# Optimization experiments

Measured on AMD Instinct MI355X. Metric: run time of the kernel, lower is better.

## Reference

```python
import jax, jax.numpy as jnp
import numpy as np

D_MODEL = 1024
D_FF = 4096
N_EXPERTS = 8
TOP_K = 2
BATCH = 4
SEQ = 2048


def setup_inputs() -> dict:
    key = jax.random.key(0)
    k0, k1, k2, k3, k4 = jax.random.split(key, 5)
    x = jax.random.normal(k0, (BATCH, SEQ, D_MODEL), dtype=jnp.float32)
    # MLP router: Linear(d,d) + bias, Tanh, Linear(d,E) no bias
    Wg1 = jax.random.normal(k1, (D_MODEL, D_MODEL), dtype=jnp.float32) * (1.0 / np.sqrt(D_MODEL))
    bg1 = jnp.zeros((D_MODEL,), dtype=jnp.float32)
    Wg2 = jax.random.normal(k2, (D_MODEL, N_EXPERTS), dtype=jnp.float32) * (1.0 / np.sqrt(D_MODEL))
    # ParallelExperts weights: [E, in, out] (bias=False)
    W1 = jax.random.normal(k3, (N_EXPERTS, D_MODEL, D_FF), dtype=jnp.float32) * 0.02
    W2 = jax.random.normal(k4, (N_EXPERTS, D_FF, D_MODEL), dtype=jnp.float32) * 0.02
    return {"x": x, "Wg1": Wg1, "bg1": bg1, "Wg2": Wg2, "W1": W1, "W2": W2}


def reference(x, Wg1, bg1, Wg2, W1, W2):
    B, L, d = x.shape
    T = B * L
    xf = x.reshape(T, d)

    # ---- top-k gating (eval mode: no noise, no dropout, no skip_mask) ----
    logits = jnp.tanh(xf @ Wg1 + bg1) @ Wg2          # [T, E]
    probs = jax.nn.softmax(logits, axis=-1)          # [T, E]
    top_k_gates, top_k_idx = jax.lax.top_k(probs, TOP_K)
    top_k_gates = top_k_gates / (top_k_gates.sum(axis=-1, keepdims=True) + 1e-6)
    # dense gate matrix: gates[t, e] = normalized gate if e selected for token t else 0
    gates = jnp.zeros_like(probs).at[jnp.arange(T)[:, None], top_k_idx].set(top_k_gates)

    # ---- expert FFNs + gate-weighted combine ----
    # Mathematically identical to scatter-dispatch/grouped-GEMM/index_add combine:
    # y_t = sum_e gates[t,e] * (gelu(x_t @ W1_e) @ W2_e); unselected experts have gate 0.
    # Scan over the small fixed expert axis to avoid an [E, T, d_ff] intermediate.
    def body(y, scanned):
        w1, w2, g = scanned                           # [d,h], [h,d], [T]
        h = jax.nn.gelu(xf @ w1)                      # [T, h]
        return y + (h @ w2) * g[:, None], None

    y0 = jnp.zeros((T, d), dtype=x.dtype)
    y, _ = jax.lax.scan(body, y0, (W1, W2, gates.T))

    # all aux-loss coefficients default to 0 -> loss is 0
    loss = jnp.asarray(0.0, dtype=x.dtype)
    return y.reshape(B, L, d), loss
```

## Files before the change

kernel.cpp:

```cpp
#include <hip/hip_runtime.h>
#include <hip/hip_bf16.h>
#include <math.h>

#define T_TOK 8192
#define DM 1024
#define DFF 4096
#define NE 8
#define HROWS 16512
#define MAX_TILES 136
#define TPX 17

#define NB_SPLIT (T_TOK * DM / 4 / 256)
#define NB_TW1 ((DFF / 32) * (DM / 32) * NE)
#define NB_TW2 ((DM / 32) * (DFF / 32) * NE)
#define NB_TSW ((DM / 32) * (DM / 32))
#define NB_ZY 8193
#define NB_ZLOG 64
#define NB_ZMETA 1
#define NB_PREP (NB_SPLIT + NB_TW1 + NB_TW2 + NB_TSW + NB_ZY + NB_ZLOG + NB_ZMETA)

typedef __attribute__((ext_vector_type(8))) short bf16x8;
typedef __attribute__((ext_vector_type(4))) float f32x4;
typedef __attribute__((ext_vector_type(8))) _Float16 f16x8;
typedef __attribute__((ext_vector_type(4))) _Float16 f16x4;

__device__ __forceinline__ void async16(const void* g, void* l) {
  __builtin_amdgcn_global_load_lds((const __attribute__((address_space(1))) void*)g,
                                   (__attribute__((address_space(3))) void*)l, 16, 0, 0);
}

__device__ __forceinline__ unsigned short f2b(float f) {
  __hip_bfloat16 h = __float2bfloat16(f);
  return *reinterpret_cast<unsigned short*>(&h);
}

__device__ __forceinline__ float tanh_fast(float z) {
  return 1.f - 2.f / (__expf(2.f * z) + 1.f);
}

__device__ __forceinline__ float gelu_fast(float v) {
  float u = v + 0.044715f * v * v * v;
  return v / (1.f + __expf(-1.5957691216057308f * u));
}

__global__ __launch_bounds__(256) void prep_all_kernel(
    const float* __restrict__ x, unsigned short* __restrict__ xb,
    _Float16* __restrict__ xh, _Float16* __restrict__ xl,
    const float* __restrict__ W1, unsigned short* __restrict__ w1t,
    const float* __restrict__ W2, unsigned short* __restrict__ w2t,
    const float* __restrict__ Wg1, _Float16* __restrict__ wth, _Float16* __restrict__ wtl,
    float* __restrict__ y, int out_size, float* __restrict__ logits, int* __restrict__ meta) {
  __shared__ float tile[32][33];
  const int b = blockIdx.x;
  const int tid = threadIdx.x;

  if (b < NB_SPLIT) {
    int i = b * 256 + tid;
    float4 v = reinterpret_cast<const float4*>(x)[i];
    ushort4 ob;
    f16x4 oh, ol;
    float f, hf;
    f = v.x; oh[0] = (_Float16)f; hf = (float)oh[0]; ol[0] = (_Float16)((f - hf) * 2048.0f); ob.x = f2b(f);
    f = v.y; oh[1] = (_Float16)f; hf = (float)oh[1]; ol[1] = (_Float16)((f - hf) * 2048.0f); ob.y = f2b(f);
    f = v.z; oh[2] = (_Float16)f; hf = (float)oh[2]; ol[2] = (_Float16)((f - hf) * 2048.0f); ob.z = f2b(f);
    f = v.w; oh[3] = (_Float16)f; hf = (float)oh[3]; ol[3] = (_Float16)((f - hf) * 2048.0f); ob.w = f2b(f);
    reinterpret_cast<ushort4*>(xb)[i] = ob;
    reinterpret_cast<f16x4*>(xh)[i] = oh;
    reinterpret_cast<f16x4*>(xl)[i] = ol;
    return;
  }

  if (b >= NB_SPLIT + NB_TW1 + NB_TW2 + NB_TSW) {
    int zb = b - (NB_SPLIT + NB_TW1 + NB_TW2 + NB_TSW);
    if (zb < NB_ZY) {
      int i4 = zb * 256 + tid;
      if ((i4 + 1) * 4 <= out_size) {
        reinterpret_cast<float4*>(y)[i4] = make_float4(0.f, 0.f, 0.f, 0.f);
      } else {
#pragma unroll
        for (int k = 0; k < 4; k++) {
          int idx = i4 * 4 + k;
          if (idx < out_size) y[idx] = 0.f;
        }
      }
    } else if (zb < NB_ZY + NB_ZLOG) {
      int i4 = (zb - NB_ZY) * 256 + tid;
      reinterpret_cast<float4*>(logits)[i4] = make_float4(0.f, 0.f, 0.f, 0.f);
    } else {
      if (tid < 16) meta[tid] = 0;
    }
    return;
  }

  const int tx = tid & 31, ty = tid >> 5;

  if (b < NB_SPLIT + NB_TW1) {
    int idx = b - NB_SPLIT;
    int e = idx >> 12, rem = idx & 4095;
    int by = rem >> 7, bx = rem & 127;
    int r0 = by * 32, c0 = bx * 32;
    const float* src = W1 + (size_t)e * DM * DFF;
    unsigned short* dst = w1t + (size_t)e * DM * DFF;
#pragma unroll
    for (int i = 0; i < 32; i += 8) tile[ty + i][tx] = src[(size_t)(r0 + ty + i) * DFF + c0 + tx];
    __syncthreads();
#pragma unroll
    for (int i = 0; i < 32; i += 8) dst[(size_t)(c0 + ty + i) * DM + r0 + tx] = f2b(tile[tx][ty + i]);
    return;
  }

  if (b < NB_SPLIT + NB_TW1 + NB_TW2) {
    int idx = b - NB_SPLIT - NB_TW1;
    int e = idx >> 12, rem = idx & 4095;
    int by = rem >> 5, bx = rem & 31;
    int r0 = by * 32, c0 = bx * 32;
    const float* src = W2 + (size_t)e * DFF * DM;
    unsigned short* dst = w2t + (size_t)e * DFF * DM;
#pragma unroll
    for (int i = 0; i < 32; i += 8) tile[ty + i][tx] = src[(size_t)(r0 + ty + i) * DM + c0 + tx];
    __syncthreads();
#pragma unroll
    for (int i = 0; i < 32; i += 8) dst[(size_t)(c0 + ty + i) * DFF + r0 + tx] = f2b(tile[tx][ty + i]);
    return;
  }

  {
    int idx = b - NB_SPLIT - NB_TW1 - NB_TW2;
    int by = idx >> 5, bx = idx & 31;
    int r0 = by * 32, c0 = bx * 32;
#pragma unroll
    for (int i = 0; i < 32; i += 8) tile[ty + i][tx] = Wg1[(size_t)(r0 + ty + i) * DM + c0 + tx];
    __syncthreads();
#pragma unroll
    for (int i = 0; i < 32; i += 8) {
      float f = tile[tx][ty + i];
      _Float16 h = (_Float16)f;
      size_t idx2 = (size_t)(c0 + ty + i) * DM + r0 + tx;
      wth[idx2] = h;
      wtl[idx2] = (_Float16)((f - (float)h) * 2048.0f);
    }
  }
}

__global__ __launch_bounds__(256) void router_mfma_kernel(
    const _Float16* __restrict__ xh, const _Float16* __restrict__ xl,
    const _Float16* __restrict__ wth, const _Float16* __restrict__ wtl,
    const float* __restrict__ bg1, const float* __restrict__ Wg2,
    float* __restrict__ logits) {
  __shared__ __align__(16) char AB[2][32768];
  __shared__ float lgt[128 * 2 * NE];

  const int tid = threadIdx.x;
  const int lane = tid & 63;
  const int w = tid >> 6;
  const int n0 = blockIdx.x * 128, m0 = blockIdx.y * 128;

  const int r0 = w * 16 + (lane >> 2);
  const int r1 = r0 + 64;
  const int sp = lane & 3;
  const int k0s = (sp ^ ((r0 >> 1) & 3)) * 8;
  const int k1s = (sp ^ ((r1 >> 1) & 3)) * 8;

  const _Float16* gAh0 = xh + (size_t)(m0 + r0) * DM + k0s;
  const _Float16* gAh1 = xh + (size_t)(m0 + r1) * DM + k1s;
  const _Float16* gAl0 = xl + (size_t)(m0 + r0) * DM + k0s;
  const _Float16* gAl1 = xl + (size_t)(m0 + r1) * DM + k1s;
  const _Float16* gBh0 = wth + (size_t)(n0 + r0) * DM + k0s;
  const _Float16* gBh1 = wth + (size_t)(n0 + r1) * DM + k1s;
  const _Float16* gBl0 = wtl + (size_t)(n0 + r0) * DM + k0s;
  const _Float16* gBl1 = wtl + (size_t)(n0 + r1) * DM + k1s;

  const int wr = (w >> 1) * 64, wc = (w & 1) * 64;
  const int l15 = lane & 15, ls = lane >> 4;

  f32x4 zero = {0.f, 0.f, 0.f, 0.f};
  f32x4 acc_hh[4][4], acc_c[4][4];
#pragma unroll
  for (int i = 0; i < 4; i++)
#pragma unroll
    for (int j = 0; j < 4; j++) { acc_hh[i][j] = zero; acc_c[i][j] = zero; }

  auto stage = [&](int buf, int kt) {
    char* b = &AB[buf][0] + w * 1024;
    async16(gAh0 + kt, b);
    async16(gAh1 + kt, b + 4096);
    async16(gAl0 + kt, b + 8192);
    async16(gAl1 + kt, b + 8192 + 4096);
    async16(gBh0 + kt, b + 16384);
    async16(gBh1 + kt, b + 16384 + 4096);
    async16(gBl0 + kt, b + 24576);
    async16(gBl1 + kt, b + 24576 + 4096);
  };
  auto computeTile = [&](int cur) {
    const char* base = &AB[cur][0];
    f16x8 ah[4], bh[4], tmp[4];
#pragma unroll
    for (int i = 0; i < 4; i++) {
      int ar = wr + i * 16 + l15;
      ah[i] = *(const f16x8*)(base + ar * 64 + ((ls ^ ((ar >> 1) & 3)) << 4));
    }
#pragma unroll
    for (int j = 0; j < 4; j++) {
      int br = wc + j * 16 + l15;
      bh[j] = *(const f16x8*)(base + 16384 + br * 64 + ((ls ^ ((br >> 1) & 3)) << 4));
    }
    __builtin_amdgcn_s_setprio(1);
#pragma unroll
    for (int i = 0; i < 4; i++)
#pragma unroll
      for (int j = 0; j < 4; j++)
        acc_hh[i][j] = __builtin_amdgcn_mfma_f32_16x16x32_f16(ah[i], bh[j], acc_hh[i][j], 0, 0, 0);
    __builtin_amdgcn_s_setprio(0);
#pragma unroll
    for (int j = 0; j < 4; j++) {
      int br = wc + j * 16 + l15;
      tmp[j] = *(const f16x8*)(base + 24576 + br * 64 + ((ls ^ ((br >> 1) & 3)) << 4));
    }
    __builtin_amdgcn_s_setprio(1);
#pragma unroll
    for (int i = 0; i < 4; i++)
#pragma unroll
      for (int j = 0; j < 4; j++)
        acc_c[i][j] = __builtin_amdgcn_mfma_f32_16x16x32_f16(ah[i], tmp[j], acc_c[i][j], 0, 0, 0);
    __builtin_amdgcn_s_setprio(0);
#pragma unroll
    for (int i = 0; i < 4; i++) {
      int ar = wr + i * 16 + l15;
      tmp[i] = *(const f16x8*)(base + 8192 + ar * 64 + ((ls ^ ((ar >> 1) & 3)) << 4));
    }
    __builtin_amdgcn_s_setprio(1);
#pragma unroll
    for (int i = 0; i < 4; i++)
#pragma unroll
      for (int j = 0; j < 4; j++)
        acc_c[i][j] = __builtin_amdgcn_mfma_f32_16x16x32_f16(tmp[i], bh[j], acc_c[i][j], 0, 0, 0);
    __builtin_amdgcn_s_setprio(0);
  };

  const int NIT = DM / 32;
  stage(0, 0);
  __syncthreads();
#pragma unroll 2
  for (int t = 0; t < NIT - 1; t++) {
    const int cur = t & 1;
    stage(cur ^ 1, (t + 1) * 32);
    computeTile(cur);
    __syncthreads();
  }
  computeTile((NIT - 1) & 1);

  float w2r[4][8];
  float bias[4];
#pragma unroll
  for (int j = 0; j < 4; j++) {
    int gn = n0 + wc + j * 16 + l15;
    bias[j] = bg1[gn];
    float4 u = *(const float4*)(Wg2 + (size_t)gn * NE);
    float4 v = *(const float4*)(Wg2 + (size_t)gn * NE + 4);
    w2r[j][0] = u.x; w2r[j][1] = u.y; w2r[j][2] = u.z; w2r[j][3] = u.w;
    w2r[j][4] = v.x; w2r[j][5] = v.y; w2r[j][6] = v.z; w2r[j][7] = v.w;
  }
  const float inv2k = 1.0f / 2048.0f;
  const int half = wc >> 6;
  const bool b3 = (l15 & 8) != 0, b2 = (l15 & 4) != 0, b1 = (l15 & 2) != 0;
#pragma unroll
  for (int i = 0; i < 4; i++) {
#pragma unroll
    for (int r = 0; r < 4; r++) {
      float s[8] = {0.f, 0.f, 0.f, 0.f, 0.f, 0.f, 0.f, 0.f};
#pragma unroll
      for (int j = 0; j < 4; j++) {
        float hv = tanh_fast(acc_hh[i][j][r] + acc_c[i][j][r] * inv2k + bias[j]);
#pragma unroll
        for (int e = 0; e < NE; e++) s[e] = fmaf(hv, w2r[j][e], s[e]);
      }
      float t4_[4], t2_[2], t1_;
#pragma unroll
      for (int q = 0; q < 4; q++) {
        float snd = b3 ? s[q] : s[q + 4];
        float rcv = __shfl_xor(snd, 8);
        t4_[q] = (b3 ? s[q + 4] : s[q]) + rcv;
      }
#pragma unroll
      for (int q = 0; q < 2; q++) {
        float snd = b2 ? t4_[q] : t4_[q + 2];
        float rcv = __shfl_xor(snd, 4);
        t2_[q] = (b2 ? t4_[q + 2] : t4_[q]) + rcv;
      }
      {
        float snd = b1 ? t2_[0] : t2_[1];
        float rcv = __shfl_xor(snd, 2);
        t1_ = (b1 ? t2_[1] : t2_[0]) + rcv;
      }
      t1_ += __shfl_xor(t1_, 1);
      int m = wr + i * 16 + ls * 4 + r;
      if (!(l15 & 1)) lgt[m * (2 * NE) + half * NE + (l15 >> 1)] = t1_;
    }
  }
  __syncthreads();
#pragma unroll
  for (int q = 0; q < 4; q++) {
    int idx = tid * 4 + q;
    int m = idx >> 3, e = idx & 7;
    float v = lgt[m * (2 * NE) + e] + lgt[m * (2 * NE) + NE + e];
    atomicAdd(&logits[(size_t)(m0 + m) * NE + e], v);
  }
}

__global__ __launch_bounds__(256) void topk_small_kernel(
    const float* __restrict__ logits, int* __restrict__ tIdx, float* __restrict__ tGate,
    int* __restrict__ counts) {
  __shared__ int lc[NE];
  const int tid = threadIdx.x;
  if (tid < NE) lc[tid] = 0;
  __syncthreads();
  int t = blockIdx.x * 256 + tid;
  float p[NE];
  float4 p0 = *(const float4*)(logits + (size_t)t * NE);
  float4 p1 = *(const float4*)(logits + (size_t)t * NE + 4);
  p[0] = p0.x; p[1] = p0.y; p[2] = p0.z; p[3] = p0.w;
  p[4] = p1.x; p[5] = p1.y; p[6] = p1.z; p[7] = p1.w;
  float v1 = -1e30f, v2 = -1e30f; int i1 = 0, i2 = 1;
#pragma unroll
  for (int e = 0; e < NE; e++) {
    float v = p[e];
    if (v > v1) { v2 = v1; i2 = i1; v1 = v; i1 = e; }
    else if (v > v2) { v2 = v; i2 = e; }
  }
  float mx = v1;
  float s = 0.f;
#pragma unroll
  for (int e = 0; e < NE; e++) s += __expf(p[e] - mx);
  float inv = 1.f / s;
  float g1 = __expf(p[i1] - mx) * inv;
  float g2 = __expf(p[i2] - mx) * inv;
  float den = 1.f / (g1 + g2 + 1e-6f);
  tIdx[2 * t] = i1; tIdx[2 * t + 1] = i2;
  tGate[2 * t] = g1 * den; tGate[2 * t + 1] = g2 * den;
  atomicAdd(&lc[i1], 1);
  atomicAdd(&lc[i2], 1);
  __syncthreads();
  if (tid < NE) atomicAdd(&counts[tid], lc[tid]);
}

__global__ void build_tiles_kernel(const int* __restrict__ counts, int* __restrict__ offsets,
                                   int4* __restrict__ desc, int* __restrict__ nTiles) {
  if (threadIdx.x != 0 || blockIdx.x != 0) return;
  int off = 0, nt = 0;
  for (int e = 0; e < NE; e++) {
    offsets[e] = off;
    int c = counts[e];
    if (c < 0) c = 0;
    if (c > 2 * T_TOK) c = 2 * T_TOK;
    for (int r = 0; r < c && nt < MAX_TILES; r += 128) {
      int v = c - r; if (v > 128) v = 128;
      desc[nt++] = make_int4(e, off + r, v, 0);
    }
    off += c;
    if (off > 2 * T_TOK) off = 2 * T_TOK;
  }
  offsets[NE] = off;
  *nTiles = nt;
}

__global__ void scatter_kernel(const int* __restrict__ tIdx, const float* __restrict__ tGate,
                               const int* __restrict__ offsets, int* __restrict__ fill,
                               int* __restrict__ tokList, float* __restrict__ gateList) {
  int id = blockIdx.x * blockDim.x + threadIdx.x;
  if (id >= 2 * T_TOK) return;
  int e = tIdx[id] & 7;
  int pos = atomicAdd(&fill[e], 1);
  int row = offsets[e] + pos;
  if (row < 0 || row >= 2 * T_TOK) return;
  tokList[row] = id >> 1;
  gateList[row] = tGate[id];
}

__global__ __launch_bounds__(256) void ffn1_kernel(
    const unsigned short* __restrict__ xb, const unsigned short* __restrict__ w1t,
    const int* __restrict__ tokList, const int4* __restrict__ desc,
    const int* __restrict__ nTiles, unsigned short* __restrict__ h) {
  const int g = blockIdx.x;
  const int tileIdx = (g & 7) * TPX + ((g >> 3) % TPX);
  const int nb = g / (8 * TPX);
  if (tileIdx >= *nTiles) return;
  int4 d = desc[tileIdx];
  const int e = d.x, rowStart = d.y, valid = d.z;
  const int n0 = nb * 128;

  __shared__ __align__(16) char AB[3][16384];

  const int tid = threadIdx.x;
  const int lane = tid & 63;
  const int w = tid >> 6;

  const int r0 = w * 16 + (lane >> 2);
  const int r1 = r0 + 64;
  const int sp = lane & 3;
  const int k0s = (sp ^ ((r0 >> 1) & 3)) * 8;
  const int k1s = (sp ^ ((r1 >> 1) & 3)) * 8;

  const unsigned short* gA0 = xb + (size_t)(tokList[rowStart + r0] & (T_TOK - 1)) * DM + k0s;
  const unsigned short* gA1 = xb + (size_t)(tokList[rowStart + r1] & (T_TOK - 1)) * DM + k1s;
  const unsigned short* gB0 = w1t + ((size_t)e * DFF + n0 + r0) * DM + k0s;
  const unsigned short* gB1 = w1t + ((size_t)e * DFF + n0 + r1) * DM + k1s;

  const int wr = (w >> 1) * 64, wc = (w & 1) * 64;
  const int l15 = lane & 15, ls = lane >> 4;

  f32x4 zero = {0.f, 0.f, 0.f, 0.f};
  f32x4 acc[4][4];
#pragma unroll
  for (int i = 0; i < 4; i++)
#pragma unroll
    for (int j = 0; j < 4; j++) acc[i][j] = zero;

  auto stage = [&](int buf, int kt) {
    char* dA = &AB[buf][0] + w * 1024;
    char* dB = dA + 8192;
    async16(gA0 + kt, dA);
    async16(gA1 + kt, dA + 4096);
    async16(gB0 + kt, dB);
    async16(gB1 + kt, dB + 4096);
  };
  auto computeTile = [&](int cur) {
    const char* rA = &AB[cur][0];
    const char* rB = rA + 8192;
    bf16x8 af[4], bfv[4];
#pragma unroll
    for (int i = 0; i < 4; i++) {
      int ar = wr + i * 16 + l15;
      af[i] = *(const bf16x8*)(rA + ar * 64 + ((ls ^ ((ar >> 1) & 3)) << 4));
    }
#pragma unroll
    for (int j = 0; j < 4; j++) {
      int br = wc + j * 16 + l15;
      bfv[j] = *(const bf16x8*)(rB + br * 64 + ((ls ^ ((br >> 1) & 3)) << 4));
    }
    __builtin_amdgcn_s_setprio(1);
#pragma unroll
    for (int i = 0; i < 4; i++)
#pragma unroll
      for (int j = 0; j < 4; j++)
        acc[i][j] = __builtin_amdgcn_mfma_f32_16x16x32_bf16(af[i], bfv[j], acc[i][j], 0, 0, 0);
    __builtin_amdgcn_s_setprio(0);
  };

  const int NIT = DM / 32;
  stage(0, 0);
  stage(1, 32);
  int cur = 0, stg = 2;
  for (int t = 0; t < NIT; t++) {
    if (t < NIT - 1) asm volatile("s_waitcnt vmcnt(4)" ::: "memory");
    else             asm volatile("s_waitcnt vmcnt(0)" ::: "memory");
    __builtin_amdgcn_s_barrier();
    __builtin_amdgcn_sched_barrier(0);
    if (t < NIT - 2) {
      stage(stg, (t + 2) * 32);
      stg = (stg == 2) ? 0 : stg + 1;
    }
    computeTile(cur);
    cur = (cur == 2) ? 0 : cur + 1;
  }

#pragma unroll
  for (int i = 0; i < 4; i++) {
#pragma unroll
    for (int r = 0; r < 4; r++) {
      int m = wr + i * 16 + ls * 4 + r;
      if (m < valid) {
        size_t base = (size_t)(rowStart + m) * DFF + n0 + wc;
#pragma unroll
        for (int j = 0; j < 4; j++) {
          h[base + j * 16 + l15] = f2b(gelu_fast(acc[i][j][r]));
        }
      }
    }
  }
}

__global__ __launch_bounds__(256) void ffn2_kernel(
    const unsigned short* __restrict__ h, const unsigned short* __restrict__ w2t,
    const int* __restrict__ tokList, const float* __restrict__ gateList,
    const int4* __restrict__ desc, const int* __restrict__ nTiles,
    float* __restrict__ y) {
  const int g = blockIdx.x;
  const int tileIdx = (g & 7) * TPX + ((g >> 3) % TPX);
  const int nb = g / (8 * TPX);
  if (tileIdx >= *nTiles) return;
  int4 d = desc[tileIdx];
  const int e = d.x, rowStart = d.y, valid = d.z;
  const int n0 = nb * 128;

  __shared__ __align__(16) char AB[3][16384];

  const int tid = threadIdx.x;
  const int lane = tid & 63;
  const int w = tid >> 6;

  const int r0 = w * 16 + (lane >> 2);
  const int r1 = r0 + 64;
  const int sp = lane & 3;
  const int k0s = (sp ^ ((r0 >> 1) & 3)) * 8;
  const int k1s = (sp ^ ((r1 >> 1) & 3)) * 8;

  const unsigned short* gA0 = h + (size_t)(rowStart + r0) * DFF + k0s;
  const unsigned short* gA1 = h + (size_t)(rowStart + r1) * DFF + k1s;
  const unsigned short* gB0 = w2t + ((size_t)e * DM + n0 + r0) * DFF + k0s;
  const unsigned short* gB1 = w2t + ((size_t)e * DM + n0 + r1) * DFF + k1s;

  const int wr = (w >> 1) * 64, wc = (w & 1) * 64;
  const int l15 = lane & 15, ls = lane >> 4;

  f32x4 zero = {0.f, 0.f, 0.f, 0.f};
  f32x4 acc[4][4];
#pragma unroll
  for (int i = 0; i < 4; i++)
#pragma unroll
    for (int j = 0; j < 4; j++) acc[i][j] = zero;

  auto stage = [&](int buf, int kt) {
    char* dA = &AB[buf][0] + w * 1024;
    char* dB = dA + 8192;
    async16(gA0 + kt, dA);
    async16(gA1 + kt, dA + 4096);
    async16(gB0 + kt, dB);
    async16(gB1 + kt, dB + 4096);
  };
  auto computeTile = [&](int cur) {
    const char* rA = &AB[cur][0];
    const char* rB = rA + 8192;
    bf16x8 af[4], bfv[4];
#pragma unroll
    for (int i = 0; i < 4; i++) {
      int ar = wr + i * 16 + l15;
      af[i] = *(const bf16x8*)(rA + ar * 64 + ((ls ^ ((ar >> 1) & 3)) << 4));
    }
#pragma unroll
    for (int j = 0; j < 4; j++) {
      int br = wc + j * 16 + l15;
      bfv[j] = *(const bf16x8*)(rB + br * 64 + ((ls ^ ((br >> 1) & 3)) << 4));
    }
    __builtin_amdgcn_s_setprio(1);
#pragma unroll
    for (int i = 0; i < 4; i++)
#pragma unroll
      for (int j = 0; j < 4; j++)
        acc[i][j] = __builtin_amdgcn_mfma_f32_16x16x32_bf16(af[i], bfv[j], acc[i][j], 0, 0, 0);
    __builtin_amdgcn_s_setprio(0);
  };

  const int NIT = DFF / 32;
  stage(0, 0);
  stage(1, 32);
  int cur = 0, stg = 2;
  for (int t = 0; t < NIT; t++) {
    if (t < NIT - 1) asm volatile("s_waitcnt vmcnt(4)" ::: "memory");
    else             asm volatile("s_waitcnt vmcnt(0)" ::: "memory");
    __builtin_amdgcn_s_barrier();
    __builtin_amdgcn_sched_barrier(0);
    if (t < NIT - 2) {
      stage(stg, (t + 2) * 32);
      stg = (stg == 2) ? 0 : stg + 1;
    }
    computeTile(cur);
    cur = (cur == 2) ? 0 : cur + 1;
  }

#pragma unroll
  for (int i = 0; i < 4; i++) {
#pragma unroll
    for (int r = 0; r < 4; r++) {
      int m = wr + i * 16 + ls * 4 + r;
      if (m < valid) {
        int row = rowStart + m;
        int tok = tokList[row] & (T_TOK - 1);
        float g2 = gateList[row];
        float* yr = y + (size_t)tok * DM + n0 + wc;
#pragma unroll
        for (int j = 0; j < 4; j++) {
          atomicAdd(&yr[j * 16 + l15], g2 * acc[i][j][r]);
        }
      }
    }
  }
}

extern "C" void kernel_launch(void* const* d_in, const int* in_sizes, int n_in,
                              void* d_out, int out_size, void* d_ws, size_t ws_size,
                              hipStream_t stream) {
  const float* x   = (const float*)d_in[0];
  const float* Wg1 = (const float*)d_in[1];
  const float* bg1 = (const float*)d_in[2];
  const float* Wg2 = (const float*)d_in[3];
  const float* W1  = (const float*)d_in[4];
  const float* W2  = (const float*)d_in[5];
  float* y = (float*)d_out;
  char* ws = (char*)d_ws;

  const size_t SZ_W1T = (size_t)NE * DFF * DM * 2;
  const size_t OFF_W1T = 0;
  const size_t OFF_W2T = OFF_W1T + SZ_W1T;
  const size_t OFF_XB  = OFF_W2T + SZ_W1T;
  const size_t OFF_H   = OFF_XB + (size_t)T_TOK * DM * 2;
  const size_t OFF_TOK = OFF_H + (size_t)HROWS * DFF * 2;
  const size_t OFF_GATE = OFF_TOK + (size_t)HROWS * 4;
  const size_t OFF_TIDX = OFF_GATE + (size_t)HROWS * 4;
  const size_t OFF_TG   = OFF_TIDX + (size_t)2 * T_TOK * 4;
  const size_t OFF_LOG  = OFF_TG + (size_t)2 * T_TOK * 4;
  const size_t OFF_META = OFF_LOG + (size_t)T_TOK * NE * 4;
  const size_t NEED = OFF_META + 4096;

  const size_t OFF_XH  = OFF_H;
  const size_t OFF_XL  = OFF_XH + (size_t)T_TOK * DM * 2;
  const size_t OFF_WTH = OFF_XL + (size_t)T_TOK * DM * 2;
  const size_t OFF_WTL = OFF_WTH + (size_t)DM * DM * 2;

  if (ws_size < NEED) {
    hipMemsetAsync(d_out, 0, (size_t)out_size * 4, stream);
    return;
  }

  unsigned short* w1t = (unsigned short*)(ws + OFF_W1T);
  unsigned short* w2t = (unsigned short*)(ws + OFF_W2T);
  unsigned short* xb  = (unsigned short*)(ws + OFF_XB);
  unsigned short* h   = (unsigned short*)(ws + OFF_H);
  _Float16* xh        = (_Float16*)(ws + OFF_XH);
  _Float16* xl        = (_Float16*)(ws + OFF_XL);
  _Float16* wth       = (_Float16*)(ws + OFF_WTH);
  _Float16* wtl       = (_Float16*)(ws + OFF_WTL);
  int* tokList        = (int*)(ws + OFF_TOK);
  float* gateList     = (float*)(ws + OFF_GATE);
  int* tIdx           = (int*)(ws + OFF_TIDX);
  float* tGate        = (float*)(ws + OFF_TG);
  float* logits       = (float*)(ws + OFF_LOG);
  int* meta           = (int*)(ws + OFF_META);
  int* counts         = (int*)(ws + OFF_META);
  int* fill           = (int*)(ws + OFF_META + 32);
  int* offsets        = (int*)(ws + OFF_META + 64);
  int* nTiles         = (int*)(ws + OFF_META + 128);
  int4* desc          = (int4*)(ws + OFF_META + 160);

  prep_all_kernel<<<dim3(NB_PREP), dim3(256), 0, stream>>>(
      x, xb, xh, xl, W1, w1t, W2, w2t, Wg1, wth, wtl, y, out_size, logits, meta);

  router_mfma_kernel<<<dim3(DM / 128, T_TOK / 128), dim3(256), 0, stream>>>(xh, xl, wth, wtl,
                                                                            bg1, Wg2, logits);
  topk_small_kernel<<<dim3(T_TOK / 256), dim3(256), 0, stream>>>(logits, tIdx, tGate, counts);
  build_tiles_kernel<<<dim3(1), dim3(64), 0, stream>>>(counts, offsets, desc, nTiles);
  scatter_kernel<<<dim3((2 * T_TOK) / 256), dim3(256), 0, stream>>>(tIdx, tGate, offsets, fill,
                                                                    tokList, gateList);

  ffn1_kernel<<<dim3((DFF / 128) * MAX_TILES), dim3(256), 0, stream>>>(xb, w1t, tokList, desc,
                                                                       nTiles, h);
  ffn2_kernel<<<dim3((DM / 128) * MAX_TILES), dim3(256), 0, stream>>>(h, w2t, tokList, gateList,
                                                                      desc, nTiles, y);
}
```

Measured before the change: 674.8 us.

## Widen expert GEMM tiles to 128x256 and split FFN2 K dimension in two

Both expert GEMM kernels now compute 128x256 output tiles instead of 128x128. Each wave holds a 64x128 accumulator, and the B-operand staging is widened to four async loads per stage. The aim is more MFMA work per LDS load and less redundant A-operand traffic. FFN2 additionally splits its 4096-long K reduction into two halves accumulated through the existing atomics, so the grid keeps enough blocks. The costs are doubled accumulator registers (lower occupancy), larger LDS use, and twice as many atomic adds on y.

```diff
diff --git a/kernel.cpp b/kernel.cpp
--- a/kernel.cpp
+++ b/kernel.cpp
@@ -386,9 +386,9 @@
   if (tileIdx >= *nTiles) return;
   int4 d = desc[tileIdx];
   const int e = d.x, rowStart = d.y, valid = d.z;
-  const int n0 = nb * 128;
-
-  __shared__ __align__(16) char AB[3][16384];
+  const int n0 = nb * 256;
+
+  __shared__ __align__(16) char AB[3][24576];
 
   const int tid = threadIdx.x;
   const int lane = tid & 63;
@@ -397,43 +397,44 @@
   const int r0 = w * 16 + (lane >> 2);
   const int r1 = r0 + 64;
   const int sp = lane & 3;
-  const int k0s = (sp ^ ((r0 >> 1) & 3)) * 8;
-  const int k1s = (sp ^ ((r1 >> 1) & 3)) * 8;
-
-  const unsigned short* gA0 = xb + (size_t)(tokList[rowStart + r0] & (T_TOK - 1)) * DM + k0s;
-  const unsigned short* gA1 = xb + (size_t)(tokList[rowStart + r1] & (T_TOK - 1)) * DM + k1s;
-  const unsigned short* gB0 = w1t + ((size_t)e * DFF + n0 + r0) * DM + k0s;
-  const unsigned short* gB1 = w1t + ((size_t)e * DFF + n0 + r1) * DM + k1s;
-
-  const int wr = (w >> 1) * 64, wc = (w & 1) * 64;
+  const int ks = (sp ^ ((r0 >> 1) & 3)) * 8;
+
+  const unsigned short* gA0 = xb + (size_t)(tokList[rowStart + r0] & (T_TOK - 1)) * DM + ks;
+  const unsigned short* gA1 = xb + (size_t)(tokList[rowStart + r1] & (T_TOK - 1)) * DM + ks;
+  const unsigned short* gB[4];
+#pragma unroll
+  for (int i = 0; i < 4; i++)
+    gB[i] = w1t + ((size_t)e * DFF + n0 + i * 64 + r0) * DM + ks;
+
+  const int wr = (w >> 1) * 64, wc = (w & 1) * 128;
   const int l15 = lane & 15, ls = lane >> 4;
 
   f32x4 zero = {0.f, 0.f, 0.f, 0.f};
-  f32x4 acc[4][4];
+  f32x4 acc[4][8];
 #pragma unroll
   for (int i = 0; i < 4; i++)
 #pragma unroll
-    for (int j = 0; j < 4; j++) acc[i][j] = zero;
+    for (int j = 0; j < 8; j++) acc[i][j] = zero;
 
   auto stage = [&](int buf, int kt) {
     char* dA = &AB[buf][0] + w * 1024;
-    char* dB = dA + 8192;
     async16(gA0 + kt, dA);
     async16(gA1 + kt, dA + 4096);
-    async16(gB0 + kt, dB);
-    async16(gB1 + kt, dB + 4096);
+    char* dB = &AB[buf][0] + 8192 + w * 1024;
+#pragma unroll
+    for (int i = 0; i < 4; i++) async16(gB[i] + kt, dB + i * 4096);
   };
   auto computeTile = [&](int cur) {
     const char* rA = &AB[cur][0];
     const char* rB = rA + 8192;
-    bf16x8 af[4], bfv[4];
+    bf16x8 af[4], bfv[8];
 #pragma unroll
     for (int i = 0; i < 4; i++) {
       int ar = wr + i * 16 + l15;
       af[i] = *(const bf16x8*)(rA + ar * 64 + ((ls ^ ((ar >> 1) & 3)) << 4));
     }
 #pragma unroll
-    for (int j = 0; j < 4; j++) {
+    for (int j = 0; j < 8; j++) {
       int br = wc + j * 16 + l15;
       bfv[j] = *(const bf16x8*)(rB + br * 64 + ((ls ^ ((br >> 1) & 3)) << 4));
     }
@@ -441,7 +442,7 @@
 #pragma unroll
     for (int i = 0; i < 4; i++)
 #pragma unroll
-      for (int j = 0; j < 4; j++)
+      for (int j = 0; j < 8; j++)
         acc[i][j] = __builtin_amdgcn_mfma_f32_16x16x32_bf16(af[i], bfv[j], acc[i][j], 0, 0, 0);
     __builtin_amdgcn_s_setprio(0);
   };
@@ -451,7 +452,7 @@
   stage(1, 32);
   int cur = 0, stg = 2;
   for (int t = 0; t < NIT; t++) {
-    if (t < NIT - 1) asm volatile("s_waitcnt vmcnt(4)" ::: "memory");
+    if (t < NIT - 1) asm volatile("s_waitcnt vmcnt(6)" ::: "memory");
     else             asm volatile("s_waitcnt vmcnt(0)" ::: "memory");
     __builtin_amdgcn_s_barrier();
     __builtin_amdgcn_sched_barrier(0);
@@ -471,7 +472,7 @@
       if (m < valid) {
         size_t base = (size_t)(rowStart + m) * DFF + n0 + wc;
 #pragma unroll
-        for (int j = 0; j < 4; j++) {
+        for (int j = 0; j < 8; j++) {
           h[base + j * 16 + l15] = f2b(gelu_fast(acc[i][j][r]));
         }
       }
@@ -486,13 +487,16 @@
     float* __restrict__ y) {
   const int g = blockIdx.x;
   const int tileIdx = (g & 7) * TPX + ((g >> 3) % TPX);
-  const int nb = g / (8 * TPX);
+  const int q = g / (8 * TPX);
+  const int nb = q & 3;
+  const int kslice = q >> 2;
   if (tileIdx >= *nTiles) return;
   int4 d = desc[tileIdx];
   const int e = d.x, rowStart = d.y, valid = d.z;
-  const int n0 = nb * 128;
-
-  __shared__ __align__(16) char AB[3][16384];
+  const int n0 = nb * 256;
+  const int kb = kslice * (DFF / 2);
+
+  __shared__ __align__(16) char AB[3][24576];
 
   const int tid = threadIdx.x;
   const int lane = tid & 63;
@@ -501,43 +505,44 @@
   const int r0 = w * 16 + (lane >> 2);
   const int r1 = r0 + 64;
   const int sp = lane & 3;
-  const int k0s = (sp ^ ((r0 >> 1) & 3)) * 8;
-  const int k1s = (sp ^ ((r1 >> 1) & 3)) * 8;
-
-  const unsigned short* gA0 = h + (size_t)(rowStart + r0) * DFF + k0s;
-  const unsigned short* gA1 = h + (size_t)(rowStart + r1) * DFF + k1s;
-  const unsigned short* gB0 = w2t + ((size_t)e * DM + n0 + r0) * DFF + k0s;
-  const unsigned short* gB1 = w2t + ((size_t)e * DM + n0 + r1) * DFF + k1s;
-
-  const int wr = (w >> 1) * 64, wc = (w & 1) * 64;
+  const int ks = (sp ^ ((r0 >> 1) & 3)) * 8;
+
+  const unsigned short* gA0 = h + (size_t)(rowStart + r0) * DFF + kb + ks;
+  const unsigned short* gA1 = h + (size_t)(rowStart + r1) * DFF + kb + ks;
+  const unsigned short* gB[4];
+#pragma unroll
+  for (int i = 0; i < 4; i++)
+    gB[i] = w2t + ((size_t)e * DM + n0 + i * 64 + r0) * DFF + kb + ks;
+
+  const int wr = (w >> 1) * 64, wc = (w & 1) * 128;
   const int l15 = lane & 15, ls = lane >> 4;
 
   f32x4 zero = {0.f, 0.f, 0.f, 0.f};
-  f32x4 acc[4][4];
+  f32x4 acc[4][8];
 #pragma unroll
   for (int i = 0; i < 4; i++)
 #pragma unroll
-    for (int j = 0; j < 4; j++) acc[i][j] = zero;
+    for (int j = 0; j < 8; j++) acc[i][j] = zero;
 
   auto stage = [&](int buf, int kt) {
     char* dA = &AB[buf][0] + w * 1024;
-    char* dB = dA + 8192;
     async16(gA0 + kt, dA);
     async16(gA1 + kt, dA + 4096);
-    async16(gB0 + kt, dB);
-    async16(gB1 + kt, dB + 4096);
+    char* dB = &AB[buf][0] + 8192 + w * 1024;
+#pragma unroll
+    for (int i = 0; i < 4; i++) async16(gB[i] + kt, dB + i * 4096);
   };
   auto computeTile = [&](int cur) {
     const char* rA = &AB[cur][0];
     const char* rB = rA + 8192;
-    bf16x8 af[4], bfv[4];
+    bf16x8 af[4], bfv[8];
 #pragma unroll
     for (int i = 0; i < 4; i++) {
       int ar = wr + i * 16 + l15;
       af[i] = *(const bf16x8*)(rA + ar * 64 + ((ls ^ ((ar >> 1) & 3)) << 4));
     }
 #pragma unroll
-    for (int j = 0; j < 4; j++) {
+    for (int j = 0; j < 8; j++) {
       int br = wc + j * 16 + l15;
       bfv[j] = *(const bf16x8*)(rB + br * 64 + ((ls ^ ((br >> 1) & 3)) << 4));
     }
@@ -545,17 +550,17 @@
 #pragma unroll
     for (int i = 0; i < 4; i++)
 #pragma unroll
-      for (int j = 0; j < 4; j++)
+      for (int j = 0; j < 8; j++)
         acc[i][j] = __builtin_amdgcn_mfma_f32_16x16x32_bf16(af[i], bfv[j], acc[i][j], 0, 0, 0);
     __builtin_amdgcn_s_setprio(0);
   };
 
-  const int NIT = DFF / 32;
+  const int NIT = (DFF / 2) / 32;
   stage(0, 0);
   stage(1, 32);
   int cur = 0, stg = 2;
   for (int t = 0; t < NIT; t++) {
-    if (t < NIT - 1) asm volatile("s_waitcnt vmcnt(4)" ::: "memory");
+    if (t < NIT - 1) asm volatile("s_waitcnt vmcnt(6)" ::: "memory");
     else             asm volatile("s_waitcnt vmcnt(0)" ::: "memory");
     __builtin_amdgcn_s_barrier();
     __builtin_amdgcn_sched_barrier(0);
@@ -578,7 +583,7 @@
         float g2 = gateList[row];
         float* yr = y + (size_t)tok * DM + n0 + wc;
 #pragma unroll
-        for (int j = 0; j < 4; j++) {
+        for (int j = 0; j < 8; j++) {
           atomicAdd(&yr[j * 16 + l15], g2 * acc[i][j][r]);
         }
       }
@@ -651,8 +656,7 @@
   scatter_kernel<<<dim3((2 * T_TOK) / 256), dim3(256), 0, stream>>>(tIdx, tGate, offsets, fill,
                                                                     tokList, gateList);
 
-  ffn1_kernel<<<dim3((DFF / 128) * MAX_TILES), dim3(256), 0, stream>>>(xb, w1t, tokList, desc,
-                                                                       nTiles, h);
-  ffn2_kernel<<<dim3((DM / 128) * MAX_TILES), dim3(256), 0, stream>>>(h, w2t, tokList, gateList,
-                                                                      desc, nTiles, y);
-}
+  ffn1_kernel<<<dim3(16 * 8 * TPX), dim3(256), 0, stream>>>(xb, w1t, tokList, desc, nTiles, h);
+  ffn2_kernel<<<dim3(8 * 8 * TPX), dim3(256), 0, stream>>>(h, w2t, tokList, gateList, desc,
+                                                           nTiles, y);
+}
```

New measurement: 703.0 us. 1.04x slower.

## Merge expert weight transposes into router kernel launch to overlap with router GEMM

Applied to the files above, without the earlier changes.

Moves the W1/W2 fp32-to-bf16 transpose blocks out of the prep kernel and appends them to the router MFMA kernel's grid. Router blocks are dispatched first and transpose blocks fill the remaining CUs, so the memory-bound transposes can run alongside the compute-bound router GEMM instead of before it. The cost is that every block in the merged kernel now reserves the router's 72KB of static LDS. That cuts how many transpose blocks can be resident per CU and may lower the bandwidth they reach.

```diff
diff --git a/kernel.cpp b/kernel.cpp
--- a/kernel.cpp
+++ b/kernel.cpp
@@ -10,14 +10,17 @@
 #define MAX_TILES 136
 #define TPX 17
 
-#define NB_SPLIT (T_TOK * DM / 4 / 256)
-#define NB_TW1 ((DFF / 32) * (DM / 32) * NE)
-#define NB_TW2 ((DM / 32) * (DFF / 32) * NE)
-#define NB_TSW ((DM / 32) * (DM / 32))
-#define NB_ZY 8193
-#define NB_ZLOG 64
-#define NB_ZMETA 1
-#define NB_PREP (NB_SPLIT + NB_TW1 + NB_TW2 + NB_TSW + NB_ZY + NB_ZLOG + NB_ZMETA)
+#define P_SPLIT 8192
+#define P_TSW 1024
+#define P_ZY 8193
+#define P_ZLOG 64
+#define P_ZMETA 1
+#define NB_PREP (P_SPLIT + P_TSW + P_ZY + P_ZLOG + P_ZMETA)
+
+#define R_ROUTER 512
+#define R_TW1 32768
+#define R_TW2 32768
+#define NB_RMEGA (R_ROUTER + R_TW1 + R_TW2)
 
 typedef __attribute__((ext_vector_type(8))) short bf16x8;
 typedef __attribute__((ext_vector_type(4))) float f32x4;
@@ -43,18 +46,16 @@
   return v / (1.f + __expf(-1.5957691216057308f * u));
 }
 
-__global__ __launch_bounds__(256) void prep_all_kernel(
+__global__ __launch_bounds__(256) void prep_small_kernel(
     const float* __restrict__ x, unsigned short* __restrict__ xb,
     _Float16* __restrict__ xh, _Float16* __restrict__ xl,
-    const float* __restrict__ W1, unsigned short* __restrict__ w1t,
-    const float* __restrict__ W2, unsigned short* __restrict__ w2t,
     const float* __restrict__ Wg1, _Float16* __restrict__ wth, _Float16* __restrict__ wtl,
     float* __restrict__ y, int out_size, float* __restrict__ logits, int* __restrict__ meta) {
   __shared__ float tile[32][33];
   const int b = blockIdx.x;
   const int tid = threadIdx.x;
 
-  if (b < NB_SPLIT) {
+  if (b < P_SPLIT) {
     int i = b * 256 + tid;
     float4 v = reinterpret_cast<const float4*>(x)[i];
     ushort4 ob;
@@ -70,64 +71,11 @@
     return;
   }
 
-  if (b >= NB_SPLIT + NB_TW1 + NB_TW2 + NB_TSW) {
-    int zb = b - (NB_SPLIT + NB_TW1 + NB_TW2 + NB_TSW);
-    if (zb < NB_ZY) {
-      int i4 = zb * 256 + tid;
-      if ((i4 + 1) * 4 <= out_size) {
-        reinterpret_cast<float4*>(y)[i4] = make_float4(0.f, 0.f, 0.f, 0.f);
-      } else {
-#pragma unroll
-        for (int k = 0; k < 4; k++) {
-          int idx = i4 * 4 + k;
-          if (idx < out_size) y[idx] = 0.f;
-        }
-      }
-    } else if (zb < NB_ZY + NB_ZLOG) {
-      int i4 = (zb - NB_ZY) * 256 + tid;
-      reinterpret_cast<float4*>(logits)[i4] = make_float4(0.f, 0.f, 0.f, 0.f);
-    } else {
-      if (tid < 16) meta[tid] = 0;
-    }
-    return;
-  }
-
-  const int tx = tid & 31, ty = tid >> 5;
-
-  if (b < NB_SPLIT + NB_TW1) {
-    int idx = b - NB_SPLIT;
-    int e = idx >> 12, rem = idx & 4095;
-    int by = rem >> 7, bx = rem & 127;
-    int r0 = by * 32, c0 = bx * 32;
-    const float* src = W1 + (size_t)e * DM * DFF;
-    unsigned short* dst = w1t + (size_t)e * DM * DFF;
-#pragma unroll
-    for (int i = 0; i < 32; i += 8) tile[ty + i][tx] = src[(size_t)(r0 + ty + i) * DFF + c0 + tx];
-    __syncthreads();
-#pragma unroll
-    for (int i = 0; i < 32; i += 8) dst[(size_t)(c0 + ty + i) * DM + r0 + tx] = f2b(tile[tx][ty + i]);
-    return;
-  }
-
-  if (b < NB_SPLIT + NB_TW1 + NB_TW2) {
-    int idx = b - NB_SPLIT - NB_TW1;
-    int e = idx >> 12, rem = idx & 4095;
-    int by = rem >> 5, bx = rem & 31;
-    int r0 = by * 32, c0 = bx * 32;
-    const float* src = W2 + (size_t)e * DFF * DM;
-    unsigned short* dst = w2t + (size_t)e * DFF * DM;
-#pragma unroll
-    for (int i = 0; i < 32; i += 8) tile[ty + i][tx] = src[(size_t)(r0 + ty + i) * DM + c0 + tx];
-    __syncthreads();
-#pragma unroll
-    for (int i = 0; i < 32; i += 8) dst[(size_t)(c0 + ty + i) * DFF + r0 + tx] = f2b(tile[tx][ty + i]);
-    return;
-  }
-
-  {
-    int idx = b - NB_SPLIT - NB_TW1 - NB_TW2;
+  if (b < P_SPLIT + P_TSW) {
+    int idx = b - P_SPLIT;
     int by = idx >> 5, bx = idx & 31;
     int r0 = by * 32, c0 = bx * 32;
+    const int tx = tid & 31, ty = tid >> 5;
 #pragma unroll
     for (int i = 0; i < 32; i += 8) tile[ty + i][tx] = Wg1[(size_t)(r0 + ty + i) * DM + c0 + tx];
     __syncthreads();
@@ -139,21 +87,75 @@
       wth[idx2] = h;
       wtl[idx2] = (_Float16)((f - (float)h) * 2048.0f);
     }
-  }
-}
-
-__global__ __launch_bounds__(256) void router_mfma_kernel(
+    return;
+  }
+
+  int zb = b - (P_SPLIT + P_TSW);
+  if (zb < P_ZY) {
+    int i4 = zb * 256 + tid;
+    if ((i4 + 1) * 4 <= out_size) {
+      reinterpret_cast<float4*>(y)[i4] = make_float4(0.f, 0.f, 0.f, 0.f);
+    } else {
+#pragma unroll
+      for (int k = 0; k < 4; k++) {
+        int idx = i4 * 4 + k;
+        if (idx < out_size) y[idx] = 0.f;
+      }
+    }
+  } else if (zb < P_ZY + P_ZLOG) {
+    int i4 = (zb - P_ZY) * 256 + tid;
+    reinterpret_cast<float4*>(logits)[i4] = make_float4(0.f, 0.f, 0.f, 0.f);
+  } else {
+    if (tid < 16) meta[tid] = 0;
+  }
+}
+
+__global__ __launch_bounds__(256) void router_mega_kernel(
     const _Float16* __restrict__ xh, const _Float16* __restrict__ xl,
     const _Float16* __restrict__ wth, const _Float16* __restrict__ wtl,
     const float* __restrict__ bg1, const float* __restrict__ Wg2,
-    float* __restrict__ logits) {
-  __shared__ __align__(16) char AB[2][32768];
-  __shared__ float lgt[128 * 2 * NE];
-
+    float* __restrict__ logits,
+    const float* __restrict__ W1, unsigned short* __restrict__ w1t,
+    const float* __restrict__ W2, unsigned short* __restrict__ w2t) {
+  __shared__ __align__(16) char smem[73728];
+  const int b = blockIdx.x;
   const int tid = threadIdx.x;
+
+  if (b >= R_ROUTER) {
+    float (*tile)[33] = (float(*)[33])smem;
+    const int tx = tid & 31, ty = tid >> 5;
+    if (b < R_ROUTER + R_TW1) {
+      int idx = b - R_ROUTER;
+      int e = idx >> 12, rem = idx & 4095;
+      int by = rem >> 7, bx = rem & 127;
+      int r0 = by * 32, c0 = bx * 32;
+      const float* src = W1 + (size_t)e * DM * DFF;
+      unsigned short* dst = w1t + (size_t)e * DM * DFF;
+#pragma unroll
+      for (int i = 0; i < 32; i += 8) tile[ty + i][tx] = src[(size_t)(r0 + ty + i) * DFF + c0 + tx];
+      __syncthreads();
+#pragma unroll
+      for (int i = 0; i < 32; i += 8) dst[(size_t)(c0 + ty + i) * DM + r0 + tx] = f2b(tile[tx][ty + i]);
+    } else {
+      int idx = b - R_ROUTER - R_TW1;
+      int e = idx >> 12, rem = idx & 4095;
+      int by = rem >> 5, bx = rem & 31;
+      int r0 = by * 32, c0 = bx * 32;
+      const float* src = W2 + (size_t)e * DFF * DM;
+      unsigned short* dst = w2t + (size_t)e * DFF * DM;
+#pragma unroll
+      for (int i = 0; i < 32; i += 8) tile[ty + i][tx] = src[(size_t)(r0 + ty + i) * DM + c0 + tx];
+      __syncthreads();
+#pragma unroll
+      for (int i = 0; i < 32; i += 8) dst[(size_t)(c0 + ty + i) * DFF + r0 + tx] = f2b(tile[tx][ty + i]);
+    }
+    return;
+  }
+
+  float* lgt = (float*)(smem + 65536);
   const int lane = tid & 63;
   const int w = tid >> 6;
-  const int n0 = blockIdx.x * 128, m0 = blockIdx.y * 128;
+  const int n0 = (b & 7) * 128, m0 = (b >> 3) * 128;
 
   const int r0 = w * 16 + (lane >> 2);
   const int r1 = r0 + 64;
@@ -181,18 +183,18 @@
     for (int j = 0; j < 4; j++) { acc_hh[i][j] = zero; acc_c[i][j] = zero; }
 
   auto stage = [&](int buf, int kt) {
-    char* b = &AB[buf][0] + w * 1024;
-    async16(gAh0 + kt, b);
-    async16(gAh1 + kt, b + 4096);
-    async16(gAl0 + kt, b + 8192);
-    async16(gAl1 + kt, b + 8192 + 4096);
-    async16(gBh0 + kt, b + 16384);
-    async16(gBh1 + kt, b + 16384 + 4096);
-    async16(gBl0 + kt, b + 24576);
-    async16(gBl1 + kt, b + 24576 + 4096);
+    char* bb = smem + buf * 32768 + w * 1024;
+    async16(gAh0 + kt, bb);
+    async16(gAh1 + kt, bb + 4096);
+    async16(gAl0 + kt, bb + 8192);
+    async16(gAl1 + kt, bb + 8192 + 4096);
+    async16(gBh0 + kt, bb + 16384);
+    async16(gBh1 + kt, bb + 16384 + 4096);
+    async16(gBl0 + kt, bb + 24576);
+    async16(gBl1 + kt, bb + 24576 + 4096);
   };
   auto computeTile = [&](int cur) {
-    const char* base = &AB[cur][0];
+    const char* base = smem + cur * 32768;
     f16x8 ah[4], bh[4], tmp[4];
 #pragma unroll
     for (int i = 0; i < 4; i++) {
@@ -641,11 +643,12 @@
   int* nTiles         = (int*)(ws + OFF_META + 128);
   int4* desc          = (int4*)(ws + OFF_META + 160);
 
-  prep_all_kernel<<<dim3(NB_PREP), dim3(256), 0, stream>>>(
-      x, xb, xh, xl, W1, w1t, W2, w2t, Wg1, wth, wtl, y, out_size, logits, meta);
-
-  router_mfma_kernel<<<dim3(DM / 128, T_TOK / 128), dim3(256), 0, stream>>>(xh, xl, wth, wtl,
-                                                                            bg1, Wg2, logits);
+  prep_small_kernel<<<dim3(NB_PREP), dim3(256), 0, stream>>>(
+      x, xb, xh, xl, Wg1, wth, wtl, y, out_size, logits, meta);
+
+  router_mega_kernel<<<dim3(NB_RMEGA), dim3(256), 0, stream>>>(
+      xh, xl, wth, wtl, bg1, Wg2, logits, W1, w1t, W2, w2t);
+
   topk_small_kernel<<<dim3(T_TOK / 256), dim3(256), 0, stream>>>(logits, tIdx, tGate, counts);
   build_tiles_kernel<<<dim3(1), dim3(64), 0, stream>>>(counts, offsets, desc, nTiles);
   scatter_kernel<<<dim3((2 * T_TOK) / 256), dim3(256), 0, stream>>>(tIdx, tGate, offsets, fill,
```

Result: slower. 730.3 us (+8.2%).

## Widen expert FFN tiles to 128x256 with 8 waves and split-K ffn2

Applied to the files above, without the earlier changes.

Both expert GEMM kernels now run 512-thread blocks computing 128x256 output tiles with 8 waves, so each gathered A tile is reused across twice as many output columns. ffn2 also splits its K=4096 reduction into two halves across separate blocks, keeping the block count up despite the wider N tile. Staging drops to three async loads per thread, and the vmcnt wait is adjusted to match. The cost is more LDS per block, which lowers occupancy, and split-K relies on the epilogue accumulating partial results into the pre-zeroed y.

```diff
diff --git a/kernel.cpp b/kernel.cpp
--- a/kernel.cpp
+++ b/kernel.cpp
@@ -376,7 +376,7 @@
   gateList[row] = tGate[id];
 }
 
-__global__ __launch_bounds__(256) void ffn1_kernel(
+__global__ __launch_bounds__(512) void ffn1_kernel(
     const unsigned short* __restrict__ xb, const unsigned short* __restrict__ w1t,
     const int* __restrict__ tokList, const int4* __restrict__ desc,
     const int* __restrict__ nTiles, unsigned short* __restrict__ h) {
@@ -386,26 +386,28 @@
   if (tileIdx >= *nTiles) return;
   int4 d = desc[tileIdx];
   const int e = d.x, rowStart = d.y, valid = d.z;
-  const int n0 = nb * 128;
-
-  __shared__ __align__(16) char AB[3][16384];
+  const int n0 = nb * 256;
+
+  __shared__ __align__(16) char AB[3][24576];
 
   const int tid = threadIdx.x;
   const int lane = tid & 63;
   const int w = tid >> 6;
 
-  const int r0 = w * 16 + (lane >> 2);
-  const int r1 = r0 + 64;
+  const int sub = lane >> 2;
   const int sp = lane & 3;
-  const int k0s = (sp ^ ((r0 >> 1) & 3)) * 8;
-  const int k1s = (sp ^ ((r1 >> 1) & 3)) * 8;
-
-  const unsigned short* gA0 = xb + (size_t)(tokList[rowStart + r0] & (T_TOK - 1)) * DM + k0s;
-  const unsigned short* gA1 = xb + (size_t)(tokList[rowStart + r1] & (T_TOK - 1)) * DM + k1s;
-  const unsigned short* gB0 = w1t + ((size_t)e * DFF + n0 + r0) * DM + k0s;
-  const unsigned short* gB1 = w1t + ((size_t)e * DFF + n0 + r1) * DM + k1s;
-
-  const int wr = (w >> 1) * 64, wc = (w & 1) * 64;
+  const int rA = w * 16 + sub;
+  const int ksA = (sp ^ ((rA >> 1) & 3)) * 8;
+  const int rB0 = w * 32 + sub;
+  const int rB1 = rB0 + 16;
+  const int ksB0 = (sp ^ ((rB0 >> 1) & 3)) * 8;
+  const int ksB1 = (sp ^ ((rB1 >> 1) & 3)) * 8;
+
+  const unsigned short* gA = xb + (size_t)(tokList[rowStart + rA] & (T_TOK - 1)) * DM + ksA;
+  const unsigned short* gB0 = w1t + ((size_t)e * DFF + n0 + rB0) * DM + ksB0;
+  const unsigned short* gB1 = w1t + ((size_t)e * DFF + n0 + rB1) * DM + ksB1;
+
+  const int wr = (w >> 2) * 64, wc = (w & 3) * 64;
   const int l15 = lane & 15, ls = lane >> 4;
 
   f32x4 zero = {0.f, 0.f, 0.f, 0.f};
@@ -416,26 +418,24 @@
     for (int j = 0; j < 4; j++) acc[i][j] = zero;
 
   auto stage = [&](int buf, int kt) {
-    char* dA = &AB[buf][0] + w * 1024;
-    char* dB = dA + 8192;
-    async16(gA0 + kt, dA);
-    async16(gA1 + kt, dA + 4096);
-    async16(gB0 + kt, dB);
-    async16(gB1 + kt, dB + 4096);
+    char* base = &AB[buf][0];
+    async16(gA + kt, base + w * 1024);
+    async16(gB0 + kt, base + 8192 + w * 2048);
+    async16(gB1 + kt, base + 8192 + w * 2048 + 1024);
   };
   auto computeTile = [&](int cur) {
-    const char* rA = &AB[cur][0];
-    const char* rB = rA + 8192;
+    const char* rAb = &AB[cur][0];
+    const char* rBb = rAb + 8192;
     bf16x8 af[4], bfv[4];
 #pragma unroll
     for (int i = 0; i < 4; i++) {
       int ar = wr + i * 16 + l15;
-      af[i] = *(const bf16x8*)(rA + ar * 64 + ((ls ^ ((ar >> 1) & 3)) << 4));
+      af[i] = *(const bf16x8*)(rAb + ar * 64 + ((ls ^ ((ar >> 1) & 3)) << 4));
     }
 #pragma unroll
     for (int j = 0; j < 4; j++) {
       int br = wc + j * 16 + l15;
-      bfv[j] = *(const bf16x8*)(rB + br * 64 + ((ls ^ ((br >> 1) & 3)) << 4));
+      bfv[j] = *(const bf16x8*)(rBb + br * 64 + ((ls ^ ((br >> 1) & 3)) << 4));
     }
     __builtin_amdgcn_s_setprio(1);
 #pragma unroll
@@ -451,7 +451,7 @@
   stage(1, 32);
   int cur = 0, stg = 2;
   for (int t = 0; t < NIT; t++) {
-    if (t < NIT - 1) asm volatile("s_waitcnt vmcnt(4)" ::: "memory");
+    if (t < NIT - 1) asm volatile("s_waitcnt vmcnt(3)" ::: "memory");
     else             asm volatile("s_waitcnt vmcnt(0)" ::: "memory");
     __builtin_amdgcn_s_barrier();
     __builtin_amdgcn_sched_barrier(0);
@@ -479,37 +479,42 @@
   }
 }
 
-__global__ __launch_bounds__(256) void ffn2_kernel(
+__global__ __launch_bounds__(512) void ffn2_kernel(
     const unsigned short* __restrict__ h, const unsigned short* __restrict__ w2t,
     const int* __restrict__ tokList, const float* __restrict__ gateList,
     const int4* __restrict__ desc, const int* __restrict__ nTiles,
     float* __restrict__ y) {
   const int g = blockIdx.x;
   const int tileIdx = (g & 7) * TPX + ((g >> 3) % TPX);
-  const int nb = g / (8 * TPX);
+  const int q = g / (8 * TPX);
+  const int nb = q & 3;
+  const int kslice = q >> 2;
   if (tileIdx >= *nTiles) return;
   int4 d = desc[tileIdx];
   const int e = d.x, rowStart = d.y, valid = d.z;
-  const int n0 = nb * 128;
-
-  __shared__ __align__(16) char AB[3][16384];
+  const int n0 = nb * 256;
+  const int kb = kslice * (DFF / 2);
+
+  __shared__ __align__(16) char AB[3][24576];
 
   const int tid = threadIdx.x;
   const int lane = tid & 63;
   const int w = tid >> 6;
 
-  const int r0 = w * 16 + (lane >> 2);
-  const int r1 = r0 + 64;
+  const int sub = lane >> 2;
   const int sp = lane & 3;
-  const int k0s = (sp ^ ((r0 >> 1) & 3)) * 8;
-  const int k1s = (sp ^ ((r1 >> 1) & 3)) * 8;
-
-  const unsigned short* gA0 = h + (size_t)(rowStart + r0) * DFF + k0s;
-  const unsigned short* gA1 = h + (size_t)(rowStart + r1) * DFF + k1s;
-  const unsigned short* gB0 = w2t + ((size_t)e * DM + n0 + r0) * DFF + k0s;
-  const unsigned short* gB1 = w2t + ((size_t)e * DM + n0 + r1) * DFF + k1s;
-
-  const int wr = (w >> 1) * 64, wc = (w & 1) * 64;
+  const int rA = w * 16 + sub;
+  const int ksA = (sp ^ ((rA >> 1) & 3)) * 8;
+  const int rB0 = w * 32 + sub;
+  const int rB1 = rB0 + 16;
+  const int ksB0 = (sp ^ ((rB0 >> 1) & 3)) * 8;
+  const int ksB1 = (sp ^ ((rB1 >> 1) & 3)) * 8;
+
+  const unsigned short* gA = h + (size_t)(rowStart + rA) * DFF + kb + ksA;
+  const unsigned short* gB0 = w2t + ((size_t)e * DM + n0 + rB0) * DFF + kb + ksB0;
+  const unsigned short* gB1 = w2t + ((size_t)e * DM + n0 + rB1) * DFF + kb + ksB1;
+
+  const int wr = (w >> 2) * 64, wc = (w & 3) * 64;
   const int l15 = lane & 15, ls = lane >> 4;
 
   f32x4 zero = {0.f, 0.f, 0.f, 0.f};
@@ -520,26 +525,24 @@
     for (int j = 0; j < 4; j++) acc[i][j] = zero;
 
   auto stage = [&](int buf, int kt) {
-    char* dA = &AB[buf][0] + w * 1024;
-    char* dB = dA + 8192;
-    async16(gA0 + kt, dA);
-    async16(gA1 + kt, dA + 4096);
-    async16(gB0 + kt, dB);
-    async16(gB1 + kt, dB + 4096);
+    char* base = &AB[buf][0];
+    async16(gA + kt, base + w * 1024);
+    async16(gB0 + kt, base + 8192 + w * 2048);
+    async16(gB1 + kt, base + 8192 + w * 2048 + 1024);
   };
   auto computeTile = [&](int cur) {
-    const char* rA = &AB[cur][0];
-    const char* rB = rA + 8192;
+    const char* rAb = &AB[cur][0];
+    const char* rBb = rAb + 8192;
     bf16x8 af[4], bfv[4];
 #pragma unroll
     for (int i = 0; i < 4; i++) {
       int ar = wr + i * 16 + l15;
-      af[i] = *(const bf16x8*)(rA + ar * 64 + ((ls ^ ((ar >> 1) & 3)) << 4));
+      af[i] = *(const bf16x8*)(rAb + ar * 64 + ((ls ^ ((ar >> 1) & 3)) << 4));
     }
 #pragma unroll
     for (int j = 0; j < 4; j++) {
       int br = wc + j * 16 + l15;
-      bfv[j] = *(const bf16x8*)(rB + br * 64 + ((ls ^ ((br >> 1) & 3)) << 4));
+      bfv[j] = *(const bf16x8*)(rBb + br * 64 + ((ls ^ ((br >> 1) & 3)) << 4));
     }
     __builtin_amdgcn_s_setprio(1);
 #pragma unroll
@@ -550,12 +553,12 @@
     __builtin_amdgcn_s_setprio(0);
   };
 
-  const int NIT = DFF / 32;
+  const int NIT = (DFF / 2) / 32;
   stage(0, 0);
   stage(1, 32);
   int cur = 0, stg = 2;
   for (int t = 0; t < NIT; t++) {
-    if (t < NIT - 1) asm volatile("s_waitcnt vmcnt(4)" ::: "memory");
+    if (t < NIT - 1) asm volatile("s_waitcnt vmcnt(3)" ::: "memory");
     else             asm volatile("s_waitcnt vmcnt(0)" ::: "memory");
     __builtin_amdgcn_s_barrier();
     __builtin_amdgcn_sched_barrier(0);
@@ -651,8 +654,7 @@
   scatter_kernel<<<dim3((2 * T_TOK) / 256), dim3(256), 0, stream>>>(tIdx, tGate, offsets, fill,
                                                                     tokList, gateList);
 
-  ffn1_kernel<<<dim3((DFF / 128) * MAX_TILES), dim3(256), 0, stream>>>(xb, w1t, tokList, desc,
-                                                                       nTiles, h);
-  ffn2_kernel<<<dim3((DM / 128) * MAX_TILES), dim3(256), 0, stream>>>(h, w2t, tokList, gateList,
-                                                                      desc, nTiles, y);
-}
+  ffn1_kernel<<<dim3(16 * 8 * TPX), dim3(512), 0, stream>>>(xb, w1t, tokList, desc, nTiles, h);
+  ffn2_kernel<<<dim3(8 * 8 * TPX), dim3(512), 0, stream>>>(h, w2t, tokList, gateList, desc,
+                                                           nTiles, y);
+}
```

Result: no change. 662.6 us (-1.8%).
